# Kernel tuning notes

Measured on AMD Instinct MI355X. Metric: run time of the kernel, lower is better.

Reference implementation:

```python
import jax, jax.numpy as jnp
import numpy as np

N_NODES = 100000
N_EDGES = 3200000
N_FEAT = 128
N_HID = 128
N_CLASS = 16
AVG_DEG = 32


def setup_inputs() -> dict:
    key = jax.random.key(0)
    ks = jax.random.split(key, 8)
    x = jax.random.normal(ks[0], (N_NODES, N_FEAT), dtype=jnp.float32)
    edge_row = jax.random.randint(ks[1], (N_EDGES,), 0, N_NODES, dtype=jnp.int32)
    edge_col = jax.random.randint(ks[2], (N_EDGES,), 0, N_NODES, dtype=jnp.int32)
    # normalized adjacency values ~ 1/degree
    edge_val = jax.random.uniform(ks[3], (N_EDGES,), dtype=jnp.float32) * (1.0 / AVG_DEG)
    W1 = jax.random.normal(ks[4], (N_FEAT, N_HID), dtype=jnp.float32) * (1.0 / np.sqrt(N_FEAT))
    b1 = jnp.zeros((N_HID,), dtype=jnp.float32)
    W4 = jax.random.normal(ks[5], (N_HID, N_CLASS), dtype=jnp.float32) * (1.0 / np.sqrt(N_HID))
    b4 = jnp.zeros((N_CLASS,), dtype=jnp.float32)
    return {"x": x, "edge_val": edge_val, "W1": W1, "b1": b1, "W4": W4, "b4": b4,
            "edge_row": edge_row, "edge_col": edge_col}


def _spmm(edge_val, edge_row, edge_col, feats, n_nodes):
    # sparse adj (COO) @ dense feats: gather source rows, scale, scatter-add to dest rows
    msgs = edge_val[:, None] * feats[edge_col]  # [E, D]
    return jax.ops.segment_sum(msgs, edge_row, num_segments=n_nodes)


def reference(x, edge_val, W1, b1, W4, b4, edge_row, edge_col):
    # gc1: adj @ (x @ W1) + b1, then ReLU (dropout is identity in eval mode)
    h = jax.nn.relu(_spmm(edge_val, edge_row, edge_col, x @ W1, N_NODES) + b1)
    # gc4: adj @ (h @ W4) + b4
    out = _spmm(edge_val, edge_row, edge_col, h @ W4, N_NODES) + b4
    return jax.nn.log_softmax(out, axis=1)
```

## Files before the change

### kernel.cpp

```cpp
#include <hip/hip_runtime.h>
#include <hip/hip_bf16.h>

constexpr int NN = 100000;
constexpr int NE = 3200000;
constexpr int NWG = 256;
constexpr int CHUNK = NE / NWG;
constexpr int CHUNK4 = CHUNK / 4;
constexpr int ROWS_B = 256;
constexpr int NBUK1 = (NN + ROWS_B - 1) / ROWS_B;
constexpr int SORT_CAP = 9216;

__device__ __forceinline__ unsigned short f2bf(float f) {
    unsigned int u = __float_as_uint(f);
    unsigned int r = (u + 0x7fffu + ((u >> 16) & 1u)) >> 16;
    return (unsigned short)r;
}

__global__ __launch_bounds__(256) void k_gemm1(const float* __restrict__ x,
                                               const float* __restrict__ W,
                                               unsigned short* __restrict__ y) {
    __shared__ float ws_[128 * 128];
    __shared__ float xs[8][128];
    const int t = threadIdx.x;
    for (int i = t; i < 128 * 128; i += 256) ws_[i] = W[i];

    const int rowg = t >> 5;
    const int cq   = (t & 31) * 4;
    const int row0 = blockIdx.x * 32;

    for (int rs = 0; rs < 32; rs += 8) {
        __syncthreads();
        {
            const int r  = t >> 5;
            const int c4 = (t & 31) * 4;
            const int row = row0 + rs + r;
            float4 val = (row < NN) ? *(const float4*)(x + row * 128 + c4)
                                    : make_float4(0.f, 0.f, 0.f, 0.f);
            *(float4*)(&xs[r][c4]) = val;
        }
        __syncthreads();
        float4 acc = make_float4(0.f, 0.f, 0.f, 0.f);
#pragma unroll
        for (int k = 0; k < 128; ++k) {
            const float xv = xs[rowg][k];
            const float4 wv = *(const float4*)(&ws_[k * 128 + cq]);
            acc.x = fmaf(xv, wv.x, acc.x);
            acc.y = fmaf(xv, wv.y, acc.y);
            acc.z = fmaf(xv, wv.z, acc.z);
            acc.w = fmaf(xv, wv.w, acc.w);
        }
        const int row = row0 + rs + rowg;
        if (row < NN) {
            ushort4 o;
            o.x = f2bf(acc.x); o.y = f2bf(acc.y);
            o.z = f2bf(acc.z); o.w = f2bf(acc.w);
            *(ushort4*)(y + row * 128 + cq) = o;
        }
    }
}


__global__ __launch_bounds__(256) void k_count(const int4* __restrict__ erow4,
                                               int* __restrict__ cnt_tbl) {
    __shared__ int hist[NBUK1];
    const int t = threadIdx.x, wg = blockIdx.x;
    for (int i = t; i < NBUK1; i += 256) hist[i] = 0;
    __syncthreads();
    const int end4 = (wg + 1) * CHUNK4;
    for (int i4 = wg * CHUNK4 + t; i4 < end4; i4 += 256) {
        const int4 r = erow4[i4];
        atomicAdd(&hist[r.x >> 8], 1);
        atomicAdd(&hist[r.y >> 8], 1);
        atomicAdd(&hist[r.z >> 8], 1);
        atomicAdd(&hist[r.w >> 8], 1);
    }
    __syncthreads();
    for (int i = t; i < NBUK1; i += 256) cnt_tbl[wg * NBUK1 + i] = hist[i];
}

__global__ __launch_bounds__(256) void k_scan2(const int* __restrict__ cnt_tbl,
                                               int* __restrict__ off_tbl,
                                               int* __restrict__ boff) {
    __shared__ int sd[256];
    const int t = threadIdx.x;
    const int b0 = 2 * t, b1 = 2 * t + 1;
    int tot = 0;
    if (b0 < NBUK1) for (int wg = 0; wg < NWG; ++wg) tot += cnt_tbl[wg * NBUK1 + b0];
    if (b1 < NBUK1) for (int wg = 0; wg < NWG; ++wg) tot += cnt_tbl[wg * NBUK1 + b1];
    sd[t] = tot;
    __syncthreads();
    for (int off = 1; off < 256; off <<= 1) {
        int a = sd[t];
        int b = (t >= off) ? sd[t - off] : 0;
        __syncthreads();
        sd[t] = a + b;
        __syncthreads();
    }
    int run = sd[t] - tot;
    if (b0 < NBUK1) {
        boff[b0] = run;
        for (int wg = 0; wg < NWG; ++wg) {
            off_tbl[wg * NBUK1 + b0] = run;
            run += cnt_tbl[wg * NBUK1 + b0];
        }
    }
    if (b1 < NBUK1) {
        boff[b1] = run;
        for (int wg = 0; wg < NWG; ++wg) {
            off_tbl[wg * NBUK1 + b1] = run;
            run += cnt_tbl[wg * NBUK1 + b1];
        }
    }
    if (t == 255) boff[NBUK1] = NE;
}

__global__ __launch_bounds__(256) void k_place(const int4* __restrict__ erow4,
                                               const int4* __restrict__ ecol4,
                                               const float4* __restrict__ eval4,
                                               const int* __restrict__ off_tbl,
                                               uint2* __restrict__ tmp) {
    __shared__ int cur[NBUK1];
    const int t = threadIdx.x, wg = blockIdx.x;
    for (int i = t; i < NBUK1; i += 256) cur[i] = off_tbl[wg * NBUK1 + i];
    __syncthreads();
    const int end4 = (wg + 1) * CHUNK4;
    for (int i4 = wg * CHUNK4 + t; i4 < end4; i4 += 256) {
        const int4 r = erow4[i4];
        const int4 c = ecol4[i4];
        const float4 v = eval4[i4];
        int p;
        p = atomicAdd(&cur[r.x >> 8], 1);
        tmp[p] = make_uint2(((unsigned)(r.x & 255) << 17) | (unsigned)c.x, __float_as_uint(v.x));
        p = atomicAdd(&cur[r.y >> 8], 1);
        tmp[p] = make_uint2(((unsigned)(r.y & 255) << 17) | (unsigned)c.y, __float_as_uint(v.y));
        p = atomicAdd(&cur[r.z >> 8], 1);
        tmp[p] = make_uint2(((unsigned)(r.z & 255) << 17) | (unsigned)c.z, __float_as_uint(v.z));
        p = atomicAdd(&cur[r.w >> 8], 1);
        tmp[p] = make_uint2(((unsigned)(r.w & 255) << 17) | (unsigned)c.w, __float_as_uint(v.w));
    }
}

__global__ __launch_bounds__(256) void k_sort2(const uint2* __restrict__ tmp,
                                               const int* __restrict__ boff,
                                               uint2* __restrict__ recs,
                                               int* __restrict__ row_start) {
    __shared__ uint2 sbuf[SORT_CAP];
    __shared__ int hist[ROWS_B];
    __shared__ int cur[ROWS_B];
    __shared__ int sd[256];
    const int b = blockIdx.x, t = threadIdx.x;
    const int base = boff[b];
    const int n = boff[b + 1] - base;
    hist[t] = 0;
    __syncthreads();
    for (int i = t; i < n; i += 256) {
        const uint2 rc = tmp[base + i];
        if (i < SORT_CAP) sbuf[i] = rc;
        atomicAdd(&hist[rc.x >> 17], 1);
    }
    __syncthreads();
    const int hv = hist[t];
    sd[t] = hv;
    __syncthreads();
    for (int off = 1; off < 256; off <<= 1) {
        int a = sd[t];
        int bb = (t >= off) ? sd[t - off] : 0;
        __syncthreads();
        sd[t] = a + bb;
        __syncthreads();
    }
    const int excl = sd[t] - hv;
    cur[t] = base + excl;
    const int gr = b * ROWS_B + t;
    if (gr < NN) row_start[gr] = base + excl;
    if (b == NBUK1 - 1 && t == 0) row_start[NN] = NE;
    __syncthreads();
    for (int i = t; i < n; i += 256) {
        const uint2 rc = (i < SORT_CAP) ? sbuf[i] : tmp[base + i];
        const int lr = rc.x >> 17;
        const int pos = atomicAdd(&cur[lr], 1);
        recs[pos] = make_uint2(rc.x & 0x1FFFFu, rc.y);
    }
}

__global__ __launch_bounds__(256) void k_spmm1(const unsigned int* __restrict__ xw1u,
                                               const int* __restrict__ row_start,
                                               const uint2* __restrict__ recs,
                                               const float* __restrict__ b1,
                                               const float* __restrict__ W4,
                                               unsigned short* __restrict__ hw4) {
    __shared__ float w4p[2048 + 48];
    __shared__ float hrow[4][132];
    const int t = threadIdx.x;
    for (int i = t; i < 2048; i += 256) {
        const int k = i >> 4;
        w4p[i + 16 * (k >> 5)] = W4[i];
    }
    __syncthreads();

    const int wid = (blockIdx.x * 256 + t) >> 6;
    const int lane = t & 63;
    if (wid >= NN) return;
    const int s = row_start[wid], e = row_start[wid + 1];
    float2 acc = make_float2(0.f, 0.f);
    for (int base = s; base < e; base += 64) {
        const int n = min(64, e - base);
        uint2 rv = make_uint2(0u, 0u);
        if (lane < n) rv = recs[base + lane];
        int j = 0;
        for (; j + 2 <= n; j += 2) {
            const int c0 = __shfl((int)rv.x, j), c1 = __shfl((int)rv.x, j + 1);
            const float v0 = __uint_as_float((unsigned int)__shfl((int)rv.y, j));
            const float v1 = __uint_as_float((unsigned int)__shfl((int)rv.y, j + 1));
            const unsigned int u0 = xw1u[c0 * 64 + lane];
            const unsigned int u1 = xw1u[c1 * 64 + lane];
            acc.x = fmaf(v0, __uint_as_float(u0 << 16), acc.x);
            acc.y = fmaf(v0, __uint_as_float(u0 & 0xffff0000u), acc.y);
            acc.x = fmaf(v1, __uint_as_float(u1 << 16), acc.x);
            acc.y = fmaf(v1, __uint_as_float(u1 & 0xffff0000u), acc.y);
        }
        if (j < n) {
            const int c0 = __shfl((int)rv.x, j);
            const float v0 = __uint_as_float((unsigned int)__shfl((int)rv.y, j));
            const unsigned int u0 = xw1u[c0 * 64 + lane];
            acc.x = fmaf(v0, __uint_as_float(u0 << 16), acc.x);
            acc.y = fmaf(v0, __uint_as_float(u0 & 0xffff0000u), acc.y);
        }
    }
    const float2 bb = *(const float2*)(b1 + (lane << 1));
    acc.x = fmaxf(acc.x + bb.x, 0.f);
    acc.y = fmaxf(acc.y + bb.y, 0.f);

    const int wv = t >> 6;
    *(float2*)(&hrow[wv][2 * lane + (lane >> 4)]) = acc;
    const int q = lane >> 4, c = lane & 15;
    float p = 0.f;
#pragma unroll
    for (int j = 0; j < 32; ++j) {
        const int k = 32 * q + j;
        p = fmaf(hrow[wv][k + q], w4p[16 * k + c + 16 * q], p);
    }
    p += __shfl_xor(p, 16);
    p += __shfl_xor(p, 32);
    if (lane < 16) hw4[wid * 16 + c] = f2bf(p);
}

__global__ __launch_bounds__(256) void k_spmm2(const __hip_bfloat16* __restrict__ hw4,
                                               const int* __restrict__ row_start,
                                               const uint2* __restrict__ recs,
                                               const float* __restrict__ b4,
                                               float* __restrict__ out) {
    const int wid = (blockIdx.x * 256 + threadIdx.x) >> 6;
    const int lane = threadIdx.x & 63;
    if (wid >= NN) return;
    const int f = lane & 15, g = lane >> 4;
    const int s = row_start[wid], e = row_start[wid + 1];
    float acc = 0.f;
    for (int base = s + g; base < e; base += 4) {
        const uint2 rv = recs[base];
        const int c = (int)rv.x;
        const float v = __uint_as_float(rv.y);
        const float a = __uint_as_float(((unsigned int)*(const unsigned short*)(hw4 + c * 16 + f)) << 16);
        acc = fmaf(v, a, acc);
    }
    acc += __shfl_xor(acc, 16);
    acc += __shfl_xor(acc, 32);
    acc += b4[f];
    float m = acc;
#pragma unroll
    for (int off = 1; off < 16; off <<= 1) m = fmaxf(m, __shfl_xor(m, off));
    const float ex = __expf(acc - m);
    float sum = ex;
#pragma unroll
    for (int off = 1; off < 16; off <<= 1) sum += __shfl_xor(sum, off);
    const float res = acc - m - __logf(sum);
    if (lane < 16) out[wid * 16 + f] = res;
}

extern "C" void kernel_launch(void* const* d_in, const int* in_sizes, int n_in,
                              void* d_out, int out_size, void* d_ws, size_t ws_size,
                              hipStream_t stream) {
    const float* x        = (const float*)d_in[0];
    const float* edge_val = (const float*)d_in[1];
    const float* W1       = (const float*)d_in[2];
    const float* b1       = (const float*)d_in[3];
    const float* W4       = (const float*)d_in[4];
    const float* b4       = (const float*)d_in[5];
    const int*   edge_row = (const int*)d_in[6];
    const int*   edge_col = (const int*)d_in[7];
    float* out = (float*)d_out;

    char* ws = (char*)d_ws;
    size_t off = 0;
    auto alloc = [&](size_t bytes) -> void* {
        void* p = ws + off;
        off = (off + bytes + 255) & ~(size_t)255;
        return p;
    };
    unsigned short* xw1 = (unsigned short*)alloc((size_t)NN * 128 * 2);
    unsigned short* hw4 = (unsigned short*)alloc((size_t)NN * 16 * 2);
    int*   cnt_tbl      = (int*)alloc((size_t)NWG * NBUK1 * 4);
    int*   off_tbl      = (int*)alloc((size_t)NWG * NBUK1 * 4);
    int*   boff         = (int*)alloc((size_t)(NBUK1 + 1) * 4);
    int*   row_start    = (int*)alloc((size_t)(NN + 1) * 4);
    uint2* tmp          = (uint2*)alloc((size_t)NE * 8);
    uint2* recs         = (uint2*)alloc((size_t)NE * 8);

    k_gemm1<<<NN / 32, 256, 0, stream>>>(x, W1, xw1);
    k_count<<<NWG, 256, 0, stream>>>((const int4*)edge_row, cnt_tbl);
    k_scan2<<<1, 256, 0, stream>>>(cnt_tbl, off_tbl, boff);
    k_place<<<NWG, 256, 0, stream>>>((const int4*)edge_row, (const int4*)edge_col,
                                     (const float4*)edge_val, off_tbl, tmp);
    k_sort2<<<NBUK1, 256, 0, stream>>>(tmp, boff, recs, row_start);
    k_spmm1<<<(NN + 3) / 4, 256, 0, stream>>>((const unsigned int*)xw1, row_start, recs,
                                              b1, W4, hw4);
    k_spmm2<<<(NN + 3) / 4, 256, 0, stream>>>((const __hip_bfloat16*)hw4, row_start, recs, b4, out);
}
```

Baseline: 536.4 us.

## Split row edges across lane groups with wide gathers in both SpMM kernels

In the first SpMM, each wavefront now splits its row's edges across four 16-lane groups. Each lane gathers a 16-byte uint4 covering eight bf16 features instead of a 4-byte word, and the partial sums are combined with cross-group shuffles. The second SpMM uses eight 8-lane groups, each lane loading two bf16 values per edge, and log-softmax works on the packed pairs. The aim is fewer, wider memory requests and more independent edge loads in flight per wavefront, replacing the per-edge shuffle broadcast loop. The cost is extra reduction shuffles, more registers, and a reworked shared-memory layout for the hidden row.

```diff
diff --git a/kernel.cpp b/kernel.cpp
--- a/kernel.cpp
+++ b/kernel.cpp
@@ -183,14 +183,14 @@
     }
 }
 
-__global__ __launch_bounds__(256) void k_spmm1(const unsigned int* __restrict__ xw1u,
+__global__ __launch_bounds__(256) void k_spmm1(const uint4* __restrict__ xw1q,
                                                const int* __restrict__ row_start,
                                                const uint2* __restrict__ recs,
-                                               const float* __restrict__ b1,
+                                               const float4* __restrict__ b1q,
                                                const float* __restrict__ W4,
                                                unsigned short* __restrict__ hw4) {
     __shared__ float w4p[2048 + 48];
-    __shared__ float hrow[4][132];
+    __shared__ float hrow[4][144];
     const int t = threadIdx.x;
     for (int i = t; i < 2048; i += 256) {
         const int k = i >> 4;
@@ -199,82 +199,94 @@
     __syncthreads();
 
     const int wid = (blockIdx.x * 256 + t) >> 6;
+    if (wid >= NN) return;
     const int lane = t & 63;
-    if (wid >= NN) return;
+    const int g = lane >> 4;
+    const int f = lane & 15;
     const int s = row_start[wid], e = row_start[wid + 1];
-    float2 acc = make_float2(0.f, 0.f);
-    for (int base = s; base < e; base += 64) {
-        const int n = min(64, e - base);
-        uint2 rv = make_uint2(0u, 0u);
-        if (lane < n) rv = recs[base + lane];
-        int j = 0;
-        for (; j + 2 <= n; j += 2) {
-            const int c0 = __shfl((int)rv.x, j), c1 = __shfl((int)rv.x, j + 1);
-            const float v0 = __uint_as_float((unsigned int)__shfl((int)rv.y, j));
-            const float v1 = __uint_as_float((unsigned int)__shfl((int)rv.y, j + 1));
-            const unsigned int u0 = xw1u[c0 * 64 + lane];
-            const unsigned int u1 = xw1u[c1 * 64 + lane];
-            acc.x = fmaf(v0, __uint_as_float(u0 << 16), acc.x);
-            acc.y = fmaf(v0, __uint_as_float(u0 & 0xffff0000u), acc.y);
-            acc.x = fmaf(v1, __uint_as_float(u1 << 16), acc.x);
-            acc.y = fmaf(v1, __uint_as_float(u1 & 0xffff0000u), acc.y);
-        }
-        if (j < n) {
-            const int c0 = __shfl((int)rv.x, j);
-            const float v0 = __uint_as_float((unsigned int)__shfl((int)rv.y, j));
-            const unsigned int u0 = xw1u[c0 * 64 + lane];
-            acc.x = fmaf(v0, __uint_as_float(u0 << 16), acc.x);
-            acc.y = fmaf(v0, __uint_as_float(u0 & 0xffff0000u), acc.y);
-        }
-    }
-    const float2 bb = *(const float2*)(b1 + (lane << 1));
-    acc.x = fmaxf(acc.x + bb.x, 0.f);
-    acc.y = fmaxf(acc.y + bb.y, 0.f);
+    float a0 = 0.f, a1 = 0.f, a2 = 0.f, a3 = 0.f, a4 = 0.f, a5 = 0.f, a6 = 0.f, a7 = 0.f;
+    for (int base = s + g; base < e; base += 4) {
+        const uint2 rv = recs[base];
+        const int c = (int)rv.x;
+        const float v = __uint_as_float(rv.y);
+        const uint4 u = xw1q[c * 16 + f];
+        a0 = fmaf(v, __uint_as_float(u.x << 16), a0);
+        a1 = fmaf(v, __uint_as_float(u.x & 0xffff0000u), a1);
+        a2 = fmaf(v, __uint_as_float(u.y << 16), a2);
+        a3 = fmaf(v, __uint_as_float(u.y & 0xffff0000u), a3);
+        a4 = fmaf(v, __uint_as_float(u.z << 16), a4);
+        a5 = fmaf(v, __uint_as_float(u.z & 0xffff0000u), a5);
+        a6 = fmaf(v, __uint_as_float(u.w << 16), a6);
+        a7 = fmaf(v, __uint_as_float(u.w & 0xffff0000u), a7);
+    }
+    a0 += __shfl_xor(a0, 16); a0 += __shfl_xor(a0, 32);
+    a1 += __shfl_xor(a1, 16); a1 += __shfl_xor(a1, 32);
+    a2 += __shfl_xor(a2, 16); a2 += __shfl_xor(a2, 32);
+    a3 += __shfl_xor(a3, 16); a3 += __shfl_xor(a3, 32);
+    a4 += __shfl_xor(a4, 16); a4 += __shfl_xor(a4, 32);
+    a5 += __shfl_xor(a5, 16); a5 += __shfl_xor(a5, 32);
+    a6 += __shfl_xor(a6, 16); a6 += __shfl_xor(a6, 32);
+    a7 += __shfl_xor(a7, 16); a7 += __shfl_xor(a7, 32);
+
+    const float4 bA = b1q[2 * f], bB = b1q[2 * f + 1];
+    a0 = fmaxf(a0 + bA.x, 0.f); a1 = fmaxf(a1 + bA.y, 0.f);
+    a2 = fmaxf(a2 + bA.z, 0.f); a3 = fmaxf(a3 + bA.w, 0.f);
+    a4 = fmaxf(a4 + bB.x, 0.f); a5 = fmaxf(a5 + bB.y, 0.f);
+    a6 = fmaxf(a6 + bB.z, 0.f); a7 = fmaxf(a7 + bB.w, 0.f);
 
     const int wv = t >> 6;
-    *(float2*)(&hrow[wv][2 * lane + (lane >> 4)]) = acc;
-    const int q = lane >> 4, c = lane & 15;
+    if (g == 0) {
+        float* hb = &hrow[wv][9 * f];
+        hb[0] = a0; hb[1] = a1; hb[2] = a2; hb[3] = a3;
+        hb[4] = a4; hb[5] = a5; hb[6] = a6; hb[7] = a7;
+    }
+    const int q = g, c = f;
     float p = 0.f;
 #pragma unroll
     for (int j = 0; j < 32; ++j) {
         const int k = 32 * q + j;
-        p = fmaf(hrow[wv][k + q], w4p[16 * k + c + 16 * q], p);
+        p = fmaf(hrow[wv][(k >> 3) * 9 + (k & 7)], w4p[528 * q + 16 * j + c], p);
     }
     p += __shfl_xor(p, 16);
     p += __shfl_xor(p, 32);
     if (lane < 16) hw4[wid * 16 + c] = f2bf(p);
 }
 
-__global__ __launch_bounds__(256) void k_spmm2(const __hip_bfloat16* __restrict__ hw4,
+__global__ __launch_bounds__(256) void k_spmm2(const unsigned int* __restrict__ hw4u,
                                                const int* __restrict__ row_start,
                                                const uint2* __restrict__ recs,
                                                const float* __restrict__ b4,
                                                float* __restrict__ out) {
     const int wid = (blockIdx.x * 256 + threadIdx.x) >> 6;
+    if (wid >= NN) return;
     const int lane = threadIdx.x & 63;
-    if (wid >= NN) return;
-    const int f = lane & 15, g = lane >> 4;
+    const int g = lane >> 3;
+    const int f2 = lane & 7;
     const int s = row_start[wid], e = row_start[wid + 1];
-    float acc = 0.f;
-    for (int base = s + g; base < e; base += 4) {
+    float ax = 0.f, ay = 0.f;
+    for (int base = s + g; base < e; base += 8) {
         const uint2 rv = recs[base];
         const int c = (int)rv.x;
         const float v = __uint_as_float(rv.y);
-        const float a = __uint_as_float(((unsigned int)*(const unsigned short*)(hw4 + c * 16 + f)) << 16);
-        acc = fmaf(v, a, acc);
-    }
-    acc += __shfl_xor(acc, 16);
-    acc += __shfl_xor(acc, 32);
-    acc += b4[f];
-    float m = acc;
-#pragma unroll
-    for (int off = 1; off < 16; off <<= 1) m = fmaxf(m, __shfl_xor(m, off));
-    const float ex = __expf(acc - m);
-    float sum = ex;
-#pragma unroll
-    for (int off = 1; off < 16; off <<= 1) sum += __shfl_xor(sum, off);
-    const float res = acc - m - __logf(sum);
-    if (lane < 16) out[wid * 16 + f] = res;
+        const unsigned int u = hw4u[c * 8 + f2];
+        ax = fmaf(v, __uint_as_float(u << 16), ax);
+        ay = fmaf(v, __uint_as_float(u & 0xffff0000u), ay);
+    }
+    ax += __shfl_xor(ax, 8);  ay += __shfl_xor(ay, 8);
+    ax += __shfl_xor(ax, 16); ay += __shfl_xor(ay, 16);
+    ax += __shfl_xor(ax, 32); ay += __shfl_xor(ay, 32);
+    const float2 bb = *(const float2*)(b4 + 2 * f2);
+    ax += bb.x; ay += bb.y;
+    float m = fmaxf(ax, ay);
+    m = fmaxf(m, __shfl_xor(m, 1));
+    m = fmaxf(m, __shfl_xor(m, 2));
+    m = fmaxf(m, __shfl_xor(m, 4));
+    float sum = __expf(ax - m) + __expf(ay - m);
+    sum += __shfl_xor(sum, 1);
+    sum += __shfl_xor(sum, 2);
+    sum += __shfl_xor(sum, 4);
+    const float lse = m + __logf(sum);
+    if (g == 0) *(float2*)(out + wid * 16 + 2 * f2) = make_float2(ax - lse, ay - lse);
 }
 
 extern "C" void kernel_launch(void* const* d_in, const int* in_sizes, int n_in,
@@ -312,7 +324,8 @@
     k_place<<<NWG, 256, 0, stream>>>((const int4*)edge_row, (const int4*)edge_col,
                                      (const float4*)edge_val, off_tbl, tmp);
     k_sort2<<<NBUK1, 256, 0, stream>>>(tmp, boff, recs, row_start);
-    k_spmm1<<<(NN + 3) / 4, 256, 0, stream>>>((const unsigned int*)xw1, row_start, recs,
-                                              b1, W4, hw4);
-    k_spmm2<<<(NN + 3) / 4, 256, 0, stream>>>((const __hip_bfloat16*)hw4, row_start, recs, b4, out);
-}
+    k_spmm1<<<(NN + 3) / 4, 256, 0, stream>>>((const uint4*)xw1, row_start, recs,
+                                              (const float4*)b1, W4, hw4);
+    k_spmm2<<<(NN + 3) / 4, 256, 0, stream>>>((const unsigned int*)hw4, row_start, recs,
+                                              b4, out);
+}
```

Result: faster. 503.9 us (-6.1%).
